# Kernel optimization log

Measured on AMD Instinct MI355X. Metric: run time of the kernel, lower is better.

## Reference

```python
import jax, jax.numpy as jnp
import numpy as np

EPS = 1e-8

def l2norm(x, axis=-1):
    norm = jnp.sqrt(jnp.sum(x * x, axis=axis, keepdims=True)) + EPS
    return x / norm


def setup_inputs() -> dict:
    key = jax.random.key(0)
    ks = jax.random.split(key, 16)
    B, N, IMG_DIM, EMBED = 256, 36, 2048, 1024
    DK = EMBED // 8  # 128
    H3 = 3 * EMBED
    r_wl = float(np.sqrt(6.0) / np.sqrt(IMG_DIM + EMBED))
    r_k = float(np.sqrt(6.0) / np.sqrt(EMBED + DK))
    r_v = float(np.sqrt(6.0) / np.sqrt(EMBED + EMBED))
    sg = 1.0 / np.sqrt(EMBED)  # torch GRU default init range
    return {
        "images": jax.random.normal(ks[0], (B, N, IMG_DIM), jnp.float32),
        "oimages": jax.random.normal(ks[1], (B, EMBED), jnp.float32),
        "wl_w": jax.random.uniform(ks[2], (EMBED, IMG_DIM), jnp.float32, -r_wl, r_wl),
        "wl_b": jnp.zeros((EMBED,), jnp.float32),
        "wk_w": jax.random.uniform(ks[3], (DK, EMBED), jnp.float32, -r_k, r_k),
        "wk_b": jnp.zeros((DK,), jnp.float32),
        "wq_w": jax.random.uniform(ks[4], (DK, EMBED), jnp.float32, -r_k, r_k),
        "wq_b": jnp.zeros((DK,), jnp.float32),
        "wv_w": jax.random.uniform(ks[5], (EMBED, EMBED), jnp.float32, -r_v, r_v),
        "wv_b": jnp.zeros((EMBED,), jnp.float32),
        "gru_wih": jax.random.uniform(ks[6], (H3, EMBED), jnp.float32, -sg, sg),
        "gru_whh": jax.random.uniform(ks[7], (H3, EMBED), jnp.float32, -sg, sg),
        "gru_bih": jax.random.uniform(ks[8], (H3,), jnp.float32, -sg, sg),
        "gru_bhh": jax.random.uniform(ks[9], (H3,), jnp.float32, -sg, sg),
    }


def gru_last_hidden(x, wih, whh, bih, bhh):
    # Single-layer batch_first GRU (torch gate order r, z, n); returns final hidden h_N.
    B, N, H = x.shape[0], x.shape[1], whh.shape[1]
    gi = jnp.einsum('bnd,gd->bng', x, wih) + bih  # (B, N, 3H), input gates precomputed

    def step(h, gi_t):
        gh = h @ whh.T + bhh
        ir, iz, inn = jnp.split(gi_t, 3, axis=-1)
        hr, hz, hn = jnp.split(gh, 3, axis=-1)
        r = jax.nn.sigmoid(ir + hr)
        z = jax.nn.sigmoid(iz + hz)
        n = jnp.tanh(inn + r * hn)
        h_new = (1.0 - z) * n + z * h
        return h_new, None

    h0 = jnp.zeros((B, H), x.dtype)
    hN, _ = jax.lax.scan(step, h0, jnp.swapaxes(gi, 0, 1))
    return hN


def reference(images, oimages, wl_w, wl_b, wk_w, wk_b, wq_w, wq_b, wv_w, wv_b,
              gru_wih, gru_whh, gru_bih, gru_bhh):
    dk = wk_w.shape[0]
    f = jnp.einsum('bni,ei->bne', images, wl_w) + wl_b      # (B, N, E)
    f = l2norm(f, axis=-1)
    f = f + oimages[:, None, :]                              # broadcast add

    k = jnp.einsum('bne,de->bnd', f, wk_w) + wk_b            # (B, N, dk)
    q = jnp.einsum('bne,de->bnd', f, wq_w) + wq_b            # (B, N, dk)
    scores = jnp.einsum('bid,bjd->bij', k, q) / jnp.sqrt(jnp.asarray(dk, f.dtype))
    w_mn = jax.nn.softmax(scores, axis=2)                    # (B, N, N)
    v = jnp.einsum('bne,de->bnd', f, wv_w) + wv_b            # (B, N, E)
    # Original torch code: (w_mn[b,i,j] * v[b,i,d]).sum(j) -> v scaled by row-sums
    # of the softmax (== 1). Expressed faithfully without the BxNxNxE intermediate:
    attn = jnp.sum(w_mn, axis=2)[..., None] * v              # == v
    f = attn + f

    hN = gru_last_hidden(f, gru_wih, gru_whh, gru_bih, gru_bhh)  # out[:, N-1, :]
    return l2norm(hN, axis=-1)
```

## Files before the change

### kernel.cpp

```cpp
#include <hip/hip_runtime.h>
#include <hip/hip_bf16.h>

#define DEVI __device__ __forceinline__

typedef short bf16x8 __attribute__((ext_vector_type(8)));
typedef float f32x4 __attribute__((ext_vector_type(4)));


DEVI unsigned short f2b(float f) {
    union { float f; unsigned u; } x; x.f = f;
    unsigned r = x.u + 0x7fffu + ((x.u >> 16) & 1u);
    return (unsigned short)(r >> 16);
}

DEVI float b2f(unsigned short u) {
    union { unsigned u; float f; } x; x.u = ((unsigned)u) << 16; return x.f;
}

DEVI void gld_lds16(const void* g, void* l) {
    __builtin_amdgcn_global_load_lds(
        (const __attribute__((address_space(1))) void*)g,
        (__attribute__((address_space(3))) void*)l, 16, 0, 0);
}

DEVI void cp_store2(void* p, unsigned short v) {
    unsigned vv = v;
    asm volatile("global_store_short %0, %1, off sc0 sc1 nt"
                 :: "v"(p), "v"(vv) : "memory");
}


__global__ __launch_bounds__(256) void cvt_f32_bf16(
    const float* __restrict__ src, unsigned short* __restrict__ dst, int n4)
{
    int stride = gridDim.x * 256;
    for (int i = blockIdx.x * 256 + threadIdx.x; i < n4; i += stride) {
        float4 v = reinterpret_cast<const float4*>(src)[i];
        ushort4 o;
        o.x = f2b(v.x); o.y = f2b(v.y); o.z = f2b(v.z); o.w = f2b(v.w);
        reinterpret_cast<ushort4*>(dst)[i] = o;
    }
}


template<int EPI>
__global__ __launch_bounds__(256) void gemm_bt(
    const unsigned short* __restrict__ A, const unsigned short* __restrict__ Bm,
    const float* __restrict__ bias, const float* resid,
    float* outF, unsigned short* outB,
    int Mn, int Nn, int K, int mtiles)
{
    __shared__ short lds[2][2][128 * 32];
    const int tid = threadIdx.x;
    const int lane = tid & 63, w = tid >> 6;
    const int bid = blockIdx.x;
    const int mt = bid % mtiles, nt = bid / mtiles;
    const int m0 = mt * 128, n0 = nt * 128;
    const int fr = lane & 15, kg = lane >> 4;
    const int wr = (w >> 1) * 64, wc = (w & 1) * 64;

    auto stage = [&](int buf, int k0) {
#pragma unroll
        for (int rnd = 0; rnd < 2; ++rnd) {
            int chunk = rnd * 256 + w * 64;
            int slot = chunk + lane;
            int row = slot >> 2, ks = slot & 3;
            gld_lds16(A + (size_t)(m0 + row) * K + k0 + ks * 8,
                      (void*)&lds[buf][0][chunk * 8]);
        }
#pragma unroll
        for (int rnd = 0; rnd < 2; ++rnd) {
            int chunk = rnd * 256 + w * 64;
            int slot = chunk + lane;
            int row = slot >> 2, ks = slot & 3;
            gld_lds16(Bm + (size_t)(n0 + row) * K + k0 + ks * 8,
                      (void*)&lds[buf][1][chunk * 8]);
        }
    };

    f32x4 acc[4][4] = {};

    stage(0, 0);
    __syncthreads();
    const int nk = K >> 5;
    for (int kt = 0; kt < nk; ++kt) {
        int buf = kt & 1;
        if (kt + 1 < nk) stage(buf ^ 1, (kt + 1) * 32);
        const short* As = lds[buf][0];
        const short* Bs = lds[buf][1];
        bf16x8 af[4], bfv[4];
#pragma unroll
        for (int m = 0; m < 4; ++m)
            af[m] = *(const bf16x8*)&As[(wr + m * 16 + fr) * 32 + kg * 8];
#pragma unroll
        for (int n = 0; n < 4; ++n)
            bfv[n] = *(const bf16x8*)&Bs[(wc + n * 16 + fr) * 32 + kg * 8];
#pragma unroll
        for (int m = 0; m < 4; ++m)
#pragma unroll
            for (int n = 0; n < 4; ++n)
                acc[m][n] = __builtin_amdgcn_mfma_f32_16x16x32_bf16(
                    af[m], bfv[n], acc[m][n], 0, 0, 0);
        __syncthreads();
    }

#pragma unroll
    for (int n = 0; n < 4; ++n) {
        int col = n0 + wc + n * 16 + fr;
        float bc = bias[col];
#pragma unroll
        for (int m = 0; m < 4; ++m) {
            f32x4 v = acc[m][n];
#pragma unroll
            for (int i = 0; i < 4; ++i) {
                int row = m0 + wr + m * 16 + kg * 4 + i;
                float val = v[i] + bc;
                if (EPI == 0) {
                    outF[(size_t)row * Nn + col] = val;
                } else if (EPI == 2) {
                    size_t idx = (size_t)row * Nn + col;
                    val += resid[idx];
                    outB[idx] = f2b(val);
                } else {
                    int b = row / 36, t = row - b * 36;
                    int g = col >> 10, cc = (col >> 4) & 63, ce = col & 15;
                    outB[((((size_t)t * 3 + g) * 64 + cc) * 16 + ce) * 256 + b]
                        = f2b(val);
                }
            }
        }
    }
}


__global__ __launch_bounds__(256) void l2norm_add(
    const float* fin, const float* __restrict__ oimg,
    float* foutF, unsigned short* __restrict__ foutB)
{
    int row = blockIdx.x;
    int b = row / 36;
    float4 v = reinterpret_cast<const float4*>(fin + (size_t)row * 1024)[threadIdx.x];
    float s = v.x * v.x + v.y * v.y + v.z * v.z + v.w * v.w;
#pragma unroll
    for (int o = 32; o; o >>= 1) s += __shfl_down(s, o, 64);
    __shared__ float ws4[4];
    int lane = threadIdx.x & 63, w = threadIdx.x >> 6;
    if (lane == 0) ws4[w] = s;
    __syncthreads();
    float tot = ws4[0] + ws4[1] + ws4[2] + ws4[3];
    float inv = 1.0f / (sqrtf(tot) + 1e-8f);
    float4 o4 = reinterpret_cast<const float4*>(oimg + (size_t)b * 1024)[threadIdx.x];
    float4 y;
    y.x = v.x * inv + o4.x; y.y = v.y * inv + o4.y;
    y.z = v.z * inv + o4.z; y.w = v.w * inv + o4.w;
    reinterpret_cast<float4*>(foutF + (size_t)row * 1024)[threadIdx.x] = y;
    ushort4 yb; yb.x = f2b(y.x); yb.y = f2b(y.y); yb.z = f2b(y.z); yb.w = f2b(y.w);
    reinterpret_cast<ushort4*>(foutB + (size_t)row * 1024)[threadIdx.x] = yb;
}


__global__ __launch_bounds__(256, 1) void gru_persist(
    const unsigned short* __restrict__ whhB,
    const unsigned short* __restrict__ giB,
    const float* __restrict__ bhh,
    unsigned short* __restrict__ hseq,
    float* __restrict__ hfin,
    unsigned* bar)
{
    __shared__ short whs[48 * 1024];
    const int tid = threadIdx.x, lane = tid & 63, w = tid >> 6;
    const int bid = blockIdx.x;
    const int c = bid >> 2, rg = bid & 3;
    const int e0 = c * 16;
    const int fr = lane & 15, kg = lane >> 4;
    const int szk = fr & 7;

    for (int it = 0; it < 24; ++it) {
        int slot = it * 256 + tid;
        int j = slot >> 7, pc = slot & 127;
        int gc = pc ^ (j & 7);
        int grow = (j >> 4) * 1024 + e0 + (j & 15);
        gld_lds16(whhB + (size_t)grow * 1024 + gc * 8, (void*)&whs[slot * 8]);
    }
    __syncthreads();

    const int e = e0 + fr;
    const float bhr = bhh[e], bhz = bhh[1024 + e], bhn = bhh[2048 + e];
    float hreg[4] = {0.f, 0.f, 0.f, 0.f};
    const int bb0 = rg * 64 + w * 16 + kg * 4;
    const int arow = rg * 64 + w * 16 + fr;
    unsigned* cnt = &bar[rg * 32];

    for (int t = 0; t < 36; ++t) {
        const unsigned short* hc = hseq + (size_t)t * 262144;
        unsigned short* hn = hseq + (size_t)(t + 1) * 262144;

        const unsigned short* hrow = hc + (size_t)arow * 1024 + kg * 8;
        bf16x8 av[32];
#pragma unroll
        for (int kt = 0; kt < 32; ++kt)
            av[kt] = *(const bf16x8*)(hrow + kt * 32);

        union { ushort4 v; unsigned short u[4]; } gv[3];
#pragma unroll
        for (int g = 0; g < 3; ++g)
            gv[g].v = *(const ushort4*)(
                giB + ((((size_t)t * 3 + g) * 64 + c) * 16 + fr) * 256 + bb0);

        f32x4 a0 = {}, a1 = {}, a2 = {};
#pragma unroll
        for (int kt = 0; kt < 32; ++kt) {
            const int pc0 = ((kt * 4 + kg) ^ szk) << 3;
            bf16x8 w0 = *(const bf16x8*)&whs[(0 * 16 + fr) * 1024 + pc0];
            a0 = __builtin_amdgcn_mfma_f32_16x16x32_bf16(av[kt], w0, a0, 0, 0, 0);
            bf16x8 w1 = *(const bf16x8*)&whs[(1 * 16 + fr) * 1024 + pc0];
            a1 = __builtin_amdgcn_mfma_f32_16x16x32_bf16(av[kt], w1, a1, 0, 0, 0);
            bf16x8 w2 = *(const bf16x8*)&whs[(2 * 16 + fr) * 1024 + pc0];
            a2 = __builtin_amdgcn_mfma_f32_16x16x32_bf16(av[kt], w2, a2, 0, 0, 0);
        }

#pragma unroll
        for (int i = 0; i < 4; ++i) {
            float ir = b2f(gv[0].u[i]), iz = b2f(gv[1].u[i]), inn = b2f(gv[2].u[i]);
            float r = 1.f / (1.f + __expf(-(ir + a0[i] + bhr)));
            float z = 1.f / (1.f + __expf(-(iz + a1[i] + bhz)));
            float n = tanhf(inn + r * (a2[i] + bhn));
            hreg[i] = (1.f - z) * n + z * hreg[i];
        }

        if (t == 35) {
#pragma unroll
            for (int i = 0; i < 4; ++i)
                hfin[(size_t)(bb0 + i) * 1024 + e] = hreg[i];
        } else {
#pragma unroll
            for (int i = 0; i < 4; ++i)
                cp_store2(&hn[(size_t)(bb0 + i) * 1024 + e], f2b(hreg[i]));
            asm volatile("s_waitcnt vmcnt(0)" ::: "memory");
            __syncthreads();
            if (tid == 0) {
                __hip_atomic_fetch_add(cnt, 1u, __ATOMIC_RELAXED,
                                       __HIP_MEMORY_SCOPE_AGENT);
                const unsigned target = 64u * (unsigned)(t + 1);
                int guard = 0;
                while (__hip_atomic_load(cnt, __ATOMIC_RELAXED,
                                         __HIP_MEMORY_SCOPE_AGENT) < target) {
                    __builtin_amdgcn_s_sleep(1);
                    if (++guard > (1 << 24)) break;
                }
            }
            __syncthreads();
        }
    }
}

__global__ __launch_bounds__(256) void zero_state(
    unsigned short* h0, unsigned* bar)
{
    int i = blockIdx.x * 256 + threadIdx.x;
    if (i < 256 * 1024) h0[i] = 0;
    if (i < 8192) bar[i] = 0;
}

__global__ __launch_bounds__(256) void final_norm(
    const float* __restrict__ hf, float* __restrict__ out)
{
    int row = blockIdx.x;
    float4 v = reinterpret_cast<const float4*>(hf + (size_t)row * 1024)[threadIdx.x];
    float s = v.x * v.x + v.y * v.y + v.z * v.z + v.w * v.w;
#pragma unroll
    for (int o = 32; o; o >>= 1) s += __shfl_down(s, o, 64);
    __shared__ float ws4[4];
    int lane = threadIdx.x & 63, w = threadIdx.x >> 6;
    if (lane == 0) ws4[w] = s;
    __syncthreads();
    float tot = ws4[0] + ws4[1] + ws4[2] + ws4[3];
    float inv = 1.0f / (sqrtf(tot) + 1e-8f);
    float4 y; y.x = v.x * inv; y.y = v.y * inv; y.z = v.z * inv; y.w = v.w * inv;
    reinterpret_cast<float4*>(out + (size_t)row * 1024)[threadIdx.x] = y;
}


extern "C" void kernel_launch(void* const* d_in, const int* in_sizes, int n_in,
                              void* d_out, int out_size, void* d_ws, size_t ws_size,
                              hipStream_t stream)
{
    constexpr int cB = 256, cN = 36, cIMG = 2048, cE = 1024, cH3 = 3072;
    constexpr int cM = cB * cN;

    const float* images  = (const float*)d_in[0];
    const float* oimages = (const float*)d_in[1];
    const float* wl_w    = (const float*)d_in[2];
    const float* wl_b    = (const float*)d_in[3];
    const float* wv_w    = (const float*)d_in[8];
    const float* wv_b    = (const float*)d_in[9];
    const float* wih     = (const float*)d_in[10];
    const float* whh     = (const float*)d_in[11];
    const float* bih     = (const float*)d_in[12];
    const float* bhh     = (const float*)d_in[13];

    char* ws = (char*)d_ws;
    size_t off = 0;
    auto alloc = [&](size_t bytes) -> char* {
        char* p = ws + off; off += (bytes + 255) & ~(size_t)255; return p;
    };
    unsigned short* imgB = (unsigned short*)alloc((size_t)cM * cIMG * 2);
    unsigned short* wlB  = (unsigned short*)alloc((size_t)cE * cIMG * 2);
    unsigned short* wvB  = (unsigned short*)alloc((size_t)cE * cE * 2);
    unsigned short* wihB = (unsigned short*)alloc((size_t)cH3 * cE * 2);
    unsigned short* whhB = (unsigned short*)alloc((size_t)cH3 * cE * 2);
    float*          fpre = (float*)alloc((size_t)cM * cE * 4);
    unsigned short* fB   = (unsigned short*)alloc((size_t)cM * cE * 2);
    unsigned short* f2B  = (unsigned short*)alloc((size_t)cM * cE * 2);
    unsigned short* giB  = (unsigned short*)alloc((size_t)cM * cH3 * 2);
    float*          hfin = (float*)alloc((size_t)cB * cE * 4);
    unsigned*       bar  = (unsigned*)alloc(8192 * 4);
    unsigned short* hseq = imgB;
    (void)ws_size;

    cvt_f32_bf16<<<2048, 256, 0, stream>>>(images, imgB, cM * cIMG / 4);
    cvt_f32_bf16<<<512, 256, 0, stream>>>(wl_w, wlB, cE * cIMG / 4);
    cvt_f32_bf16<<<256, 256, 0, stream>>>(wv_w, wvB, cE * cE / 4);
    cvt_f32_bf16<<<512, 256, 0, stream>>>(wih, wihB, cH3 * cE / 4);
    cvt_f32_bf16<<<512, 256, 0, stream>>>(whh, whhB, cH3 * cE / 4);

    gemm_bt<0><<<72 * 8, 256, 0, stream>>>(imgB, wlB, wl_b, nullptr,
                                           fpre, nullptr, cM, cE, cIMG, 72);
    l2norm_add<<<cM, 256, 0, stream>>>(fpre, oimages, fpre, fB);

    gemm_bt<2><<<72 * 8, 256, 0, stream>>>(fB, wvB, wv_b, fpre,
                                           nullptr, f2B, cM, cE, cE, 72);
    gemm_bt<3><<<72 * 24, 256, 0, stream>>>(f2B, wihB, bih, nullptr,
                                            nullptr, giB, cM, cH3, cE, 72);

    zero_state<<<1024, 256, 0, stream>>>(hseq, bar);

    void* args[] = { (void*)&whhB, (void*)&giB, (void*)&bhh, (void*)&hseq,
                     (void*)&hfin, (void*)&bar };
    hipLaunchCooperativeKernel((void*)gru_persist, dim3(256), dim3(256),
                               args, 0, stream);

    final_norm<<<cB, 256, 0, stream>>>(hfin, (float*)d_out);
}
```

Measured before the change: 816.0 us.

## Rework GRU grid barrier to per-block flags, coalesced h stores, prefetch gates

```diff
diff --git a/kernel.cpp b/kernel.cpp
--- a/kernel.cpp
+++ b/kernel.cpp
@@ -23,22 +23,47 @@
         (__attribute__((address_space(3))) void*)l, 16, 0, 0);
 }
 
-DEVI void cp_store2(void* p, unsigned short v) {
-    unsigned vv = v;
-    asm volatile("global_store_short %0, %1, off sc0 sc1 nt"
-                 :: "v"(p), "v"(vv) : "memory");
-}
-
-
-__global__ __launch_bounds__(256) void cvt_f32_bf16(
-    const float* __restrict__ src, unsigned short* __restrict__ dst, int n4)
-{
+DEVI void cp_store8(void* p, unsigned long long v) {
+    asm volatile("global_store_dwordx2 %0, %1, off sc0 sc1 nt"
+                 :: "v"(p), "v"(v) : "memory");
+}
+DEVI void cp_store4(void* p, unsigned v) {
+    asm volatile("global_store_dword %0, %1, off sc0 sc1 nt"
+                 :: "v"(p), "v"(v) : "memory");
+}
+DEVI unsigned cp_load4(const void* p) {
+    unsigned r;
+    asm volatile("global_load_dword %0, %1, off sc0 sc1 nt\n\ts_waitcnt vmcnt(0)"
+                 : "=v"(r) : "v"(p) : "memory");
+    return r;
+}
+
+
+__global__ __launch_bounds__(256) void cvt_all(
+    const float* __restrict__ im, const float* __restrict__ wl,
+    const float* __restrict__ wv, const float* __restrict__ wih,
+    const float* __restrict__ whh,
+    unsigned short* __restrict__ imB, unsigned short* __restrict__ wlB,
+    unsigned short* __restrict__ wvB, unsigned short* __restrict__ wihB,
+    unsigned short* __restrict__ whhB)
+{
+    const int T0 = 4718592;
+    const int T1 = T0 + 524288;
+    const int T2 = T1 + 262144;
+    const int T3 = T2 + 786432;
+    const int T4 = T3 + 786432;
     int stride = gridDim.x * 256;
-    for (int i = blockIdx.x * 256 + threadIdx.x; i < n4; i += stride) {
-        float4 v = reinterpret_cast<const float4*>(src)[i];
+    for (int i = blockIdx.x * 256 + threadIdx.x; i < T4; i += stride) {
+        const float* s; unsigned short* d; int j;
+        if (i < T0)      { s = im;  d = imB;  j = i; }
+        else if (i < T1) { s = wl;  d = wlB;  j = i - T0; }
+        else if (i < T2) { s = wv;  d = wvB;  j = i - T1; }
+        else if (i < T3) { s = wih; d = wihB; j = i - T2; }
+        else             { s = whh; d = whhB; j = i - T3; }
+        float4 v = reinterpret_cast<const float4*>(s)[j];
         ushort4 o;
         o.x = f2b(v.x); o.y = f2b(v.y); o.z = f2b(v.z); o.w = f2b(v.w);
-        reinterpret_cast<ushort4*>(dst)[i] = o;
+        reinterpret_cast<ushort4*>(d)[j] = o;
     }
 }
 
@@ -168,6 +193,7 @@
     unsigned* bar)
 {
     __shared__ short whs[48 * 1024];
+    __shared__ short tb[4][16][16];
     const int tid = threadIdx.x, lane = tid & 63, w = tid >> 6;
     const int bid = blockIdx.x;
     const int c = bid >> 2, rg = bid & 3;
@@ -189,7 +215,13 @@
     float hreg[4] = {0.f, 0.f, 0.f, 0.f};
     const int bb0 = rg * 64 + w * 16 + kg * 4;
     const int arow = rg * 64 + w * 16 + fr;
-    unsigned* cnt = &bar[rg * 32];
+
+    union GV { ushort4 v; unsigned short u[4]; };
+    GV gcur[3], gnxt[3];
+#pragma unroll
+    for (int g = 0; g < 3; ++g)
+        gcur[g].v = *(const ushort4*)(
+            giB + (((size_t)g * 64 + c) * 16 + fr) * 256 + bb0);
 
     for (int t = 0; t < 36; ++t) {
         const unsigned short* hc = hseq + (size_t)t * 262144;
@@ -200,12 +232,6 @@
 #pragma unroll
         for (int kt = 0; kt < 32; ++kt)
             av[kt] = *(const bf16x8*)(hrow + kt * 32);
-
-        union { ushort4 v; unsigned short u[4]; } gv[3];
-#pragma unroll
-        for (int g = 0; g < 3; ++g)
-            gv[g].v = *(const ushort4*)(
-                giB + ((((size_t)t * 3 + g) * 64 + c) * 16 + fr) * 256 + bb0);
 
         f32x4 a0 = {}, a1 = {}, a2 = {};
 #pragma unroll
@@ -221,7 +247,8 @@
 
 #pragma unroll
         for (int i = 0; i < 4; ++i) {
-            float ir = b2f(gv[0].u[i]), iz = b2f(gv[1].u[i]), inn = b2f(gv[2].u[i]);
+            float ir = b2f(gcur[0].u[i]), iz = b2f(gcur[1].u[i]),
+                  inn = b2f(gcur[2].u[i]);
             float r = 1.f / (1.f + __expf(-(ir + a0[i] + bhr)));
             float z = 1.f / (1.f + __expf(-(iz + a1[i] + bhz)));
             float n = tanhf(inn + r * (a2[i] + bhn));
@@ -235,21 +262,36 @@
         } else {
 #pragma unroll
             for (int i = 0; i < 4; ++i)
-                cp_store2(&hn[(size_t)(bb0 + i) * 1024 + e], f2b(hreg[i]));
+                tb[w][kg * 4 + i][fr] = (short)f2b(hreg[i]);
+            asm volatile("s_waitcnt lgkmcnt(0)" ::: "memory");
+            __builtin_amdgcn_sched_barrier(0);
+            {
+                int trow = lane & 15, tc4 = lane >> 4;
+                unsigned long long dv =
+                    *(const unsigned long long*)&tb[w][trow][tc4 * 4];
+                cp_store8(&hn[(size_t)(rg * 64 + w * 16 + trow) * 1024
+                              + e0 + tc4 * 4], dv);
+            }
             asm volatile("s_waitcnt vmcnt(0)" ::: "memory");
             __syncthreads();
-            if (tid == 0) {
-                __hip_atomic_fetch_add(cnt, 1u, __ATOMIC_RELAXED,
-                                       __HIP_MEMORY_SCOPE_AGENT);
-                const unsigned target = 64u * (unsigned)(t + 1);
+            if (tid == 0)
+                cp_store4(&bar[rg * 64 + c], (unsigned)(t + 1));
+#pragma unroll
+            for (int g = 0; g < 3; ++g)
+                gnxt[g].v = *(const ushort4*)(
+                    giB + ((((size_t)(t + 1) * 3 + g) * 64 + c) * 16 + fr) * 256
+                    + bb0);
+            if (w == 0) {
+                const unsigned* fp = &bar[rg * 64 + lane];
+                const unsigned tgt = (unsigned)(t + 1);
                 int guard = 0;
-                while (__hip_atomic_load(cnt, __ATOMIC_RELAXED,
-                                         __HIP_MEMORY_SCOPE_AGENT) < target) {
+                while (cp_load4(fp) < tgt) {
                     __builtin_amdgcn_s_sleep(1);
-                    if (++guard > (1 << 24)) break;
+                    if (++guard > (1 << 20)) break;
                 }
             }
             __syncthreads();
+            gcur[0] = gnxt[0]; gcur[1] = gnxt[1]; gcur[2] = gnxt[2];
         }
     }
 }
@@ -314,15 +356,12 @@
     unsigned short* f2B  = (unsigned short*)alloc((size_t)cM * cE * 2);
     unsigned short* giB  = (unsigned short*)alloc((size_t)cM * cH3 * 2);
     float*          hfin = (float*)alloc((size_t)cB * cE * 4);
+    unsigned short* hseq = (unsigned short*)alloc((size_t)36 * cB * cE * 2);
     unsigned*       bar  = (unsigned*)alloc(8192 * 4);
-    unsigned short* hseq = imgB;
     (void)ws_size;
 
-    cvt_f32_bf16<<<2048, 256, 0, stream>>>(images, imgB, cM * cIMG / 4);
-    cvt_f32_bf16<<<512, 256, 0, stream>>>(wl_w, wlB, cE * cIMG / 4);
-    cvt_f32_bf16<<<256, 256, 0, stream>>>(wv_w, wvB, cE * cE / 4);
-    cvt_f32_bf16<<<512, 256, 0, stream>>>(wih, wihB, cH3 * cE / 4);
-    cvt_f32_bf16<<<512, 256, 0, stream>>>(whh, whhB, cH3 * cE / 4);
+    cvt_all<<<2048, 256, 0, stream>>>(images, wl_w, wv_w, wih, whh,
+                                      imgB, wlB, wvB, wihB, whhB);
 
     gemm_bt<0><<<72 * 8, 256, 0, stream>>>(imgB, wlB, wl_b, nullptr,
                                            fpre, nullptr, cM, cE, cIMG, 72);
```

Result: slower. 957.6 us (+17.3%).
